# Optimization experiments

Hardware: AMD Instinct MI355X
Metric: run time of the kernel (lower is better)

## Reference

```python
import jax, jax.numpy as jnp
import numpy as np

D_MODEL = 1024
D_STATE = 16
LN_EPS = 1e-5


def setup_inputs() -> dict:
    key = jax.random.key(0)
    ks = jax.random.split(key, 10)
    B, L, D, N = 4, 1024, D_MODEL, D_STATE
    s = lambda fan_in: 1.0 / np.sqrt(fan_in)
    x_in = jax.random.normal(ks[0], (B, L, D), dtype=jnp.float32)
    W_in = jax.random.uniform(ks[1], (D, 2 * D), jnp.float32, -s(D), s(D))
    W_x = jax.random.uniform(ks[2], (D, D + 2 * N), jnp.float32, -s(D), s(D))
    W_dt = jax.random.uniform(ks[3], (D, D), jnp.float32, -s(D), s(D))
    b_dt = jax.random.uniform(ks[4], (D,), jnp.float32, -4.0, -1.0)
    A_log = jnp.tile(jnp.log(jnp.arange(1, N + 1, dtype=jnp.float32))[None, :], (D, 1))
    D_param = jnp.ones((D,), dtype=jnp.float32)
    W_out = jax.random.uniform(ks[5], (D, D), jnp.float32, -s(D), s(D))
    ln_g = jnp.ones((D,), dtype=jnp.float32)
    ln_b = jnp.zeros((D,), dtype=jnp.float32)
    return {"x_in": x_in, "W_in": W_in, "W_x": W_x, "W_dt": W_dt, "b_dt": b_dt,
            "A_log": A_log, "D_param": D_param, "W_out": W_out, "ln_g": ln_g, "ln_b": ln_b}


def reference(x_in, W_in, W_x, W_dt, b_dt, A_log, D_param, W_out, ln_g, ln_b):
    B, L, D = x_in.shape
    N = A_log.shape[1]
    xz = x_in @ W_in                       # [B,L,2D]
    x, z = xz[..., :D], xz[..., D:]
    proj = x @ W_x                         # [B,L,D+2N]
    delta_raw = proj[..., :D]
    B_ssm = proj[..., D:D + N]
    C_ssm = proj[..., D + N:]
    delta = jax.nn.softplus(delta_raw @ W_dt + b_dt)   # [B,L,D]
    A = -jnp.exp(A_log)                    # [D,N]
    dA = jnp.exp(jnp.einsum('bld,dn->bldn', delta, A))      # [B,L,D,N]
    dBx = jnp.einsum('bld,bln->bldn', delta * x, B_ssm)      # dB * x, fused

    def step(h, inp):
        dA_t, dBx_t, C_t = inp             # [B,D,N],[B,D,N],[B,N]
        h = dA_t * h + dBx_t
        y_t = jnp.einsum('bdn,bn->bd', h, C_t)
        return h, y_t

    h0 = jnp.zeros((B, D, N), dtype=x.dtype)
    xs = (jnp.moveaxis(dA, 1, 0), jnp.moveaxis(dBx, 1, 0), jnp.moveaxis(C_ssm, 1, 0))
    _, ys = jax.lax.scan(step, h0, xs)     # ys: [L,B,D]
    y = jnp.moveaxis(ys, 0, 1) + x * D_param
    y = (y * jax.nn.silu(z)) @ W_out
    res = y + x_in
    mu = jnp.mean(res, axis=-1, keepdims=True)
    var = jnp.var(res, axis=-1, keepdims=True)
    return (res - mu) * jax.lax.rsqrt(var + LN_EPS) * ln_g + ln_b
```

## Files before the change

kernel.cpp:

```cpp
#include <hip/hip_runtime.h>

#define D_MODEL 1024
#define D_STATE 16
#define M_ROWS  4096
#define SEQ_L   1024
#define NSEG    64
#define LSEG    16

typedef __bf16 bf16x8 __attribute__((ext_vector_type(8)));
typedef float  f32x4  __attribute__((ext_vector_type(4)));

__device__ __forceinline__ unsigned short f2bf(float f) {
  unsigned int u = __builtin_bit_cast(unsigned int, f);
  u += 0x7fffu + ((u >> 16) & 1u);
  return (unsigned short)(u >> 16);
}
__device__ __forceinline__ float bf2f(unsigned short b) {
  unsigned int u = ((unsigned int)b) << 16;
  return __builtin_bit_cast(float, u);
}
__device__ __forceinline__ float load_elem(const void* p, size_t i, int isbf) {
  if (isbf) return bf2f(((const unsigned short*)p)[i]);
  return ((const float*)p)[i];
}

__device__ __forceinline__ void gload16(const void* g, void* l) {
  typedef const __attribute__((address_space(1))) unsigned int GU;
  typedef __attribute__((address_space(3))) unsigned int LU;
  __builtin_amdgcn_global_load_lds((GU*)(unsigned long long)g,
                                   (LU*)(unsigned int)(unsigned long long)l,
                                   16, 0, 0);
}

__global__ void detect_kernel(const unsigned short* __restrict__ x, int* __restrict__ flag) {
  __shared__ int cnt;
  if (threadIdx.x == 0) cnt = 0;
  __syncthreads();
  unsigned int v = x[2 * threadIdx.x];
  unsigned int e = (v >> 7) & 0xFFu;
  int ok = (e >= 100u && e <= 135u) ? 1 : 0;
  atomicAdd(&cnt, ok);
  __syncthreads();
  if (threadIdx.x == 0) *flag = (cnt >= 128) ? 1 : 0;
}

__global__ void convert_x_kernel(const void* __restrict__ src,
                                 unsigned short* __restrict__ dstb,
                                 const int* __restrict__ flag) {
  int c = blockIdx.x * blockDim.x + threadIdx.x;
  int isbf = *flag;
  if (isbf) {
    ((uint4*)dstb)[c] = ((const uint4*)src)[c];
  } else {
    float4 a = ((const float4*)src)[2 * c];
    float4 b = ((const float4*)src)[2 * c + 1];
    uint4 p;
    p.x = (unsigned int)f2bf(a.x) | ((unsigned int)f2bf(a.y) << 16);
    p.y = (unsigned int)f2bf(a.z) | ((unsigned int)f2bf(a.w) << 16);
    p.z = (unsigned int)f2bf(b.x) | ((unsigned int)f2bf(b.y) << 16);
    p.w = (unsigned int)f2bf(b.z) | ((unsigned int)f2bf(b.w) << 16);
    ((uint4*)dstb)[c] = p;
  }
}

__global__ void convert_smalls_kernel(const void* b_dt, const void* A_log, const void* Dp,
                                      const void* ln_g, const void* ln_b,
                                      float* o_bdt, float* o_a2, float* o_dp,
                                      float* o_lng, float* o_lnb,
                                      const int* __restrict__ flag) {
  int g = blockIdx.x * blockDim.x + threadIdx.x;
  int isbf = *flag;
  if (g < 1024)              o_bdt[g]          = load_elem(b_dt, g, isbf);
  else if (g < 17408) {
    float v = load_elem(A_log, g - 1024, isbf);
    o_a2[g - 1024] = -expf(v) * 1.4426950408889634f;
  }
  else if (g < 18432)        o_dp[g - 17408]   = load_elem(Dp, g - 17408, isbf);
  else if (g < 19456)        o_lng[g - 18432]  = load_elem(ln_g, g - 18432, isbf);
  else                       o_lnb[g - 19456]  = load_elem(ln_b, g - 19456, isbf);
}

__global__ void transpose_all_kernel(const void* __restrict__ s0, const void* __restrict__ s1,
                                     const void* __restrict__ s2, const void* __restrict__ s3,
                                     unsigned short* __restrict__ d0, unsigned short* __restrict__ d1,
                                     unsigned short* __restrict__ d2, unsigned short* __restrict__ d3,
                                     const int* __restrict__ flag) {
  __shared__ float tile[32][33];
  const void* src; unsigned short* dst; int ncols, nx;
  switch (blockIdx.z) {
    case 0:  src = s0; dst = d0; ncols = 2048; nx = 64; break;
    case 1:  src = s1; dst = d1; ncols = 1056; nx = 33; break;
    case 2:  src = s2; dst = d2; ncols = 1024; nx = 32; break;
    default: src = s3; dst = d3; ncols = 1024; nx = 32; break;
  }
  if ((int)blockIdx.x >= nx) return;
  int tx = threadIdx.x, ty = threadIdx.y;
  int n0 = blockIdx.x * 32, k0 = blockIdx.y * 32;
  int isbf = *flag;
  #pragma unroll
  for (int r = 0; r < 4; ++r) {
    int k = k0 + ty + r * 8;
    int n = n0 + tx;
    float v = (n < ncols) ? load_elem(src, (size_t)k * ncols + n, isbf) : 0.f;
    tile[ty + r * 8][tx] = v;
  }
  __syncthreads();
  #pragma unroll
  for (int r = 0; r < 4; ++r) {
    int n = n0 + ty + r * 8;
    int k = k0 + tx;
    dst[(size_t)n * 1024 + k] = f2bf(tile[tx][ty + r * 8]);
  }
}

template<int MODE>
__global__ __launch_bounds__(256, 4) void gemm_bf(
    const unsigned short* __restrict__ A, const unsigned short* __restrict__ Bt, int ldb,
    void* __restrict__ o0, void* __restrict__ o1, void* __restrict__ o2,
    float* __restrict__ o3, float* __restrict__ o4,
    const float* __restrict__ aux, const void* __restrict__ auxv,
    const int* __restrict__ flag) {
  __shared__ __align__(16) unsigned short a_lds[3][64 * 32];
  __shared__ __align__(16) unsigned short b_lds[3][128 * 32];
  const int tid = threadIdx.x;
  const int m0 = blockIdx.x * 64, n0 = blockIdx.y * 128;
  const int wave = tid >> 6, lane = tid & 63;
  const int wr = (wave >> 1) * 32, wc = (wave & 1) * 64;
  const int lrow = lane & 15, quad = lane >> 4;

  const int sc = (lane & 3) ^ ((lane >> 3) & 3);
  const unsigned short* gA  = A  + (size_t)(m0 + wave * 16 + (lane >> 2)) * 1024 + sc * 8;
  const unsigned short* gB  = Bt + (size_t)(n0 + wave * 32 + (lane >> 2)) * ldb + sc * 8;
  const unsigned short* gB2 = gB + (size_t)16 * ldb;
  const int q2 = quad ^ ((lrow >> 1) & 3);

  f32x4 acc[2][4];
  #pragma unroll
  for (int i = 0; i < 2; ++i)
    #pragma unroll
    for (int j = 0; j < 4; ++j)
      #pragma unroll
      for (int r = 0; r < 4; ++r) acc[i][j][r] = 0.f;

  auto issue = [&](int k) {
    unsigned short* ab = a_lds[k % 3] + wave * 16 * 32;
    unsigned short* bb = b_lds[k % 3] + wave * 32 * 32;
    gload16(gA + k * 32, ab);
    gload16(gB + k * 32, bb);
    gload16(gB2 + k * 32, bb + 16 * 32);
  };
  auto compute = [&](int k) {
    const unsigned short* ard = a_lds[k % 3] + (wr + lrow) * 32 + q2 * 8;
    const unsigned short* brd = b_lds[k % 3] + (wc + lrow) * 32 + q2 * 8;
    bf16x8 af[2], bfr[4];
    #pragma unroll
    for (int i = 0; i < 2; ++i) af[i] = *(const bf16x8*)(ard + i * 16 * 32);
    #pragma unroll
    for (int j = 0; j < 4; ++j) bfr[j] = *(const bf16x8*)(brd + j * 16 * 32);
    #pragma unroll
    for (int i = 0; i < 2; ++i)
      #pragma unroll
      for (int j = 0; j < 4; ++j)
        acc[i][j] = __builtin_amdgcn_mfma_f32_16x16x32_bf16(af[i], bfr[j], acc[i][j], 0, 0, 0);
  };

  issue(0);
  issue(1);
  #pragma unroll
  for (int k = 0; k < 31; ++k) {
    asm volatile("s_waitcnt vmcnt(3)" ::: "memory");
    __builtin_amdgcn_s_barrier();
    if (k + 2 < 32) issue(k + 2);
    compute(k);
  }
  asm volatile("s_waitcnt vmcnt(0)" ::: "memory");
  __builtin_amdgcn_s_barrier();
  compute(31);

  const int isbf = (MODE == 4) ? *flag : 0;

  #pragma unroll
  for (int i = 0; i < 2; ++i) {
    #pragma unroll
    for (int jj = 0; jj < 4; ++jj) {
      #pragma unroll
      for (int r = 0; r < 4; ++r) {
        int m = m0 + wr + i * 16 + quad * 4 + r;
        int n = n0 + wc + jj * 16 + lrow;
        float v = acc[i][jj][r];
        if (MODE == 1) {
          if (n < 1024) {
            ((unsigned short*)o0)[(size_t)m * 1024 + n] = f2bf(v);
          } else {
            float sig = 1.f / (1.f + expf(-v));
            ((unsigned short*)o1)[(size_t)m * 1024 + (n - 1024)] = f2bf(v * sig);
          }
        } else if (MODE == 2) {
          if (n < 1024)       ((unsigned short*)o0)[(size_t)m * 1024 + n] = f2bf(v);
          else if (n < 1040)  o3[(size_t)m * D_STATE + (n - 1024)] = v;
          else if (n < 1056)  o4[(size_t)m * D_STATE + (n - 1040)] = v;
        } else if (MODE == 3) {
          float t = v + aux[n];
          float sp = (t > 20.f) ? t : log1pf(expf(t));
          ((unsigned short*)o0)[(size_t)m * 1024 + n] = f2bf(sp);
        } else {
          ((float*)o0)[(size_t)m * 1024 + n] =
              v + load_elem(auxv, (size_t)m * 1024 + n, isbf);
        }
      }
    }
  }
}

template<int PHASE>
__global__ __launch_bounds__(256) void scan_phase(
    const unsigned short* __restrict__ dl_bf, const unsigned short* __restrict__ x_bf,
    const unsigned short* __restrict__ z_bf, const float* __restrict__ Bs,
    const float* __restrict__ Cs, const float* __restrict__ A2g,
    const float* __restrict__ Dpar, const float* __restrict__ hinit,
    float* __restrict__ Hout, float* __restrict__ sdout,
    unsigned short* __restrict__ g) {
  __shared__ float4 bsh[LSEG][4];
  __shared__ float4 csh[LSEG][4];
  const int tid = threadIdx.x;
  const int bid = blockIdx.x;
  const int seg = bid >> 4;
  const int b = (bid >> 2) & 3;
  const int dc = bid & 3;
  const int d = dc * 256 + tid;
  const int t0 = seg * LSEG;
  const int bd = b * D_MODEL + d;

  if (tid < LSEG * 4) {
    int r = tid >> 2, q = tid & 3;
    size_t src = ((size_t)b * SEQ_L + t0 + r) * 4 + q;
    bsh[r][q] = ((const float4*)Bs)[src];
    if (PHASE == 1) csh[r][q] = ((const float4*)Cs)[src];
  }

  float A2r[16];
  {
    const float4* a4 = (const float4*)(A2g + (size_t)d * 16);
    #pragma unroll
    for (int q = 0; q < 4; ++q) {
      float4 v = a4[q];
      A2r[4*q] = v.x; A2r[4*q+1] = v.y; A2r[4*q+2] = v.z; A2r[4*q+3] = v.w;
    }
  }
  float h[16];
  if (PHASE == 1) {
    const float4* h4 = (const float4*)(hinit + (((size_t)seg * 4096) + bd) * 16);
    #pragma unroll
    for (int q = 0; q < 4; ++q) {
      float4 v = h4[q];
      h[4*q] = v.x; h[4*q+1] = v.y; h[4*q+2] = v.z; h[4*q+3] = v.w;
    }
  } else {
    #pragma unroll
    for (int n = 0; n < 16; ++n) h[n] = 0.f;
  }
  const float Dpd = (PHASE == 1) ? Dpar[d] : 0.f;
  float sd = 0.f;
  const size_t base = ((size_t)b * SEQ_L + t0) * D_MODEL + d;
  __syncthreads();

  unsigned short dreg[2][8], xreg[2][8], zreg[2][8];
  #pragma unroll
  for (int t = 0; t < 8; ++t) {
    size_t o = base + (size_t)t * D_MODEL;
    dreg[0][t] = dl_bf[o]; xreg[0][t] = x_bf[o];
    if (PHASE == 1) zreg[0][t] = z_bf[o];
  }
  #pragma unroll
  for (int c = 0; c < LSEG / 8; ++c) {
    const int cur = c & 1, nxt = cur ^ 1;
    if (c < LSEG / 8 - 1) {
      #pragma unroll
      for (int t = 0; t < 8; ++t) {
        size_t o = base + (size_t)((c + 1) * 8 + t) * D_MODEL;
        dreg[nxt][t] = dl_bf[o]; xreg[nxt][t] = x_bf[o];
        if (PHASE == 1) zreg[nxt][t] = z_bf[o];
      }
    }
    #pragma unroll
    for (int t = 0; t < 8; ++t) {
      const int tt = c * 8 + t;
      float dl = bf2f(dreg[cur][t]);
      float xx = bf2f(xreg[cur][t]);
      float dx = dl * xx;
      sd += dl;
      float4 b0 = bsh[tt][0], b1 = bsh[tt][1], b2 = bsh[tt][2], b3 = bsh[tt][3];
      float bb[16] = {b0.x,b0.y,b0.z,b0.w, b1.x,b1.y,b1.z,b1.w,
                      b2.x,b2.y,b2.z,b2.w, b3.x,b3.y,b3.z,b3.w};
      if (PHASE == 0) {
        #pragma unroll
        for (int n = 0; n < 16; ++n) {
          float dA = exp2f(dl * A2r[n]);
          h[n] = fmaf(dA, h[n], dx * bb[n]);
        }
      } else {
        float4 c0 = csh[tt][0], c1 = csh[tt][1], c2 = csh[tt][2], c3 = csh[tt][3];
        float cc[16] = {c0.x,c0.y,c0.z,c0.w, c1.x,c1.y,c1.z,c1.w,
                        c2.x,c2.y,c2.z,c2.w, c3.x,c3.y,c3.z,c3.w};
        float y = 0.f;
        #pragma unroll
        for (int n = 0; n < 16; ++n) {
          float dA = exp2f(dl * A2r[n]);
          h[n] = fmaf(dA, h[n], dx * bb[n]);
          y = fmaf(h[n], cc[n], y);
        }
        float zz = bf2f(zreg[cur][t]);
        g[base + (size_t)tt * D_MODEL] = f2bf(fmaf(xx, Dpd, y) * zz);
      }
    }
  }
  if (PHASE == 0) {
    float4* ho = (float4*)(Hout + (((size_t)seg * 4096) + bd) * 16);
    #pragma unroll
    for (int q = 0; q < 4; ++q)
      ho[q] = make_float4(h[4*q], h[4*q+1], h[4*q+2], h[4*q+3]);
    sdout[(size_t)seg * 4096 + bd] = sd;
  }
}

__global__ __launch_bounds__(256) void scan_phaseB(
    const float* __restrict__ H, const float* __restrict__ sdelta,
    const float* __restrict__ A2g, float* __restrict__ hinit) {
  int gidx = blockIdx.x * 256 + threadIdx.x;
  int bd = gidx >> 4, n = gidx & 15;
  float A2 = A2g[(size_t)(bd & (D_MODEL - 1)) * 16 + n];
  float hp = 0.f;
  for (int s = 0; s < NSEG; ++s) {
    size_t idx = ((size_t)s * 4096 + bd) * 16 + n;
    hinit[idx] = hp;
    float P = exp2f(A2 * sdelta[(size_t)s * 4096 + bd]);
    hp = fmaf(P, hp, H[idx]);
  }
}

__global__ __launch_bounds__(256) void ln_kernel(const float* __restrict__ res,
    const float* __restrict__ lng, const float* __restrict__ lnb,
    void* __restrict__ out, const int* __restrict__ flag) {
  int row = blockIdx.x, tid = threadIdx.x;
  const float4* r4 = (const float4*)(res + (size_t)row * D_MODEL);
  float4 v = r4[tid];
  float s = v.x + v.y + v.z + v.w;
  float q = v.x * v.x + v.y * v.y + v.z * v.z + v.w * v.w;
  #pragma unroll
  for (int m = 1; m < 64; m <<= 1) { s += __shfl_xor(s, m); q += __shfl_xor(q, m); }
  __shared__ float ss[4], qs[4];
  int w = tid >> 6;
  if ((tid & 63) == 0) { ss[w] = s; qs[w] = q; }
  __syncthreads();
  s = ss[0] + ss[1] + ss[2] + ss[3];
  q = qs[0] + qs[1] + qs[2] + qs[3];
  float mu = s * (1.f / D_MODEL);
  float var = q * (1.f / D_MODEL) - mu * mu;
  float rstd = rsqrtf(var + 1e-5f);
  float4 gg = ((const float4*)lng)[tid];
  float4 bb = ((const float4*)lnb)[tid];
  float o0 = (v.x - mu) * rstd * gg.x + bb.x;
  float o1 = (v.y - mu) * rstd * gg.y + bb.y;
  float o2 = (v.z - mu) * rstd * gg.z + bb.z;
  float o3 = (v.w - mu) * rstd * gg.w + bb.w;
  if (*flag) {
    ushort4 pv;
    pv.x = f2bf(o0); pv.y = f2bf(o1); pv.z = f2bf(o2); pv.w = f2bf(o3);
    ((ushort4*)out)[(size_t)row * 256 + tid] = pv;
  } else {
    ((float4*)out)[(size_t)row * 256 + tid] = make_float4(o0, o1, o2, o3);
  }
}

extern "C" void kernel_launch(void* const* d_in, const int* in_sizes, int n_in,
                              void* d_out, int out_size, void* d_ws, size_t ws_size,
                              hipStream_t stream) {
  (void)in_sizes; (void)n_in; (void)out_size; (void)ws_size;
  const void* x_in  = d_in[0];
  const void* W_in  = d_in[1];
  const void* W_x   = d_in[2];
  const void* W_dt  = d_in[3];
  const void* b_dt  = d_in[4];
  const void* A_log = d_in[5];
  const void* D_par = d_in[6];
  const void* W_out = d_in[7];
  const void* ln_g  = d_in[8];
  const void* ln_b  = d_in[9];

  char* ws = (char*)d_ws;
  size_t off = 0;
  auto alloc = [&](size_t bytes) -> void* {
    void* p = ws + off;
    off += (bytes + 255) & ~(size_t)255;
    return p;
  };
  int* flag               = (int*)alloc(16);
  unsigned short* x_in_b  = (unsigned short*)alloc((size_t)M_ROWS * D_MODEL * 2);
  float* bdt_f            = (float*)alloc(1024 * 4);
  float* a2_f             = (float*)alloc(16384 * 4);
  float* dp_f             = (float*)alloc(1024 * 4);
  float* lng_f            = (float*)alloc(1024 * 4);
  float* lnb_f            = (float*)alloc(1024 * 4);
  unsigned short* wt_in   = (unsigned short*)alloc((size_t)2048 * 1024 * 2);
  unsigned short* wt_x    = (unsigned short*)alloc((size_t)1152 * 1024 * 2);
  unsigned short* wt_dt   = (unsigned short*)alloc((size_t)1024 * 1024 * 2);
  unsigned short* wt_out  = (unsigned short*)alloc((size_t)1024 * 1024 * 2);
  unsigned short* x_bf    = (unsigned short*)alloc((size_t)M_ROWS * D_MODEL * 2);
  unsigned short* s_bf    = (unsigned short*)alloc((size_t)M_ROWS * D_MODEL * 2);
  unsigned short* draw_bf = (unsigned short*)alloc((size_t)M_ROWS * D_MODEL * 2);
  unsigned short* delta_bf= (unsigned short*)alloc((size_t)M_ROWS * D_MODEL * 2);
  float* bssm_f           = (float*)alloc((size_t)M_ROWS * D_STATE * 4);
  float* cssm_f           = (float*)alloc((size_t)M_ROWS * D_STATE * 4);
  float* H_f              = (float*)alloc((size_t)NSEG * 4096 * 16 * 4);
  float* hinit_f          = (float*)alloc((size_t)NSEG * 4096 * 16 * 4);
  float* sdelta_f         = (float*)alloc((size_t)NSEG * 4096 * 4);
  unsigned short* g_bf = draw_bf;
  float* res_f = (float*)x_bf;

  detect_kernel<<<1, 256, 0, stream>>>((const unsigned short*)x_in, flag);
  convert_x_kernel<<<2048, 256, 0, stream>>>(x_in, x_in_b, flag);
  convert_smalls_kernel<<<80, 256, 0, stream>>>(b_dt, A_log, D_par, ln_g, ln_b,
                                                bdt_f, a2_f, dp_f, lng_f, lnb_f, flag);
  dim3 tb(32, 8);
  transpose_all_kernel<<<dim3(64, 32, 4), tb, 0, stream>>>(
      W_in, W_x, W_dt, W_out, wt_in, wt_x, wt_dt, wt_out, flag);

  gemm_bf<1><<<dim3(64, 16), 256, 0, stream>>>(x_in_b, wt_in, 1024,
      x_bf, s_bf, nullptr, nullptr, nullptr, nullptr, nullptr, flag);
  gemm_bf<2><<<dim3(64, 9), 256, 0, stream>>>(x_bf, wt_x, 1024,
      draw_bf, nullptr, nullptr, bssm_f, cssm_f, nullptr, nullptr, flag);
  gemm_bf<3><<<dim3(64, 8), 256, 0, stream>>>(draw_bf, wt_dt, 1024,
      delta_bf, nullptr, nullptr, nullptr, nullptr, bdt_f, nullptr, flag);

  scan_phase<0><<<1024, 256, 0, stream>>>(delta_bf, x_bf, nullptr, bssm_f, nullptr,
                                          a2_f, nullptr, nullptr, H_f, sdelta_f, nullptr);
  scan_phaseB<<<256, 256, 0, stream>>>(H_f, sdelta_f, a2_f, hinit_f);
  scan_phase<1><<<1024, 256, 0, stream>>>(delta_bf, x_bf, s_bf, bssm_f, cssm_f,
                                          a2_f, dp_f, hinit_f, nullptr, nullptr, g_bf);

  gemm_bf<4><<<dim3(64, 8), 256, 0, stream>>>(g_bf, wt_out, 1024,
      res_f, nullptr, nullptr, nullptr, nullptr, nullptr, x_in, flag);
  ln_kernel<<<4096, 256, 0, stream>>>(res_f, lng_f, lnb_f, d_out, flag);
}
```

Baseline: 279.6 us.

## Precompute W_x·W_dt product to merge the delta GEMMs and fuse conversion kernels

Computes U = (W_x[:, :D] @ W_dt)^T once per call as a weight-only GEMM, then computes delta and the B/C projections from x in a single GEMM. This drops the separate delta_raw GEMM over all 4096 rows and its intermediate buffer. The dtype detection kernel is replaced by an inline wave ballot in each consumer, and the x and small-parameter conversions are merged into one launch. The weight product adds an extra bf16 rounding step compared with the two-stage path.

```diff
diff --git a/kernel.cpp b/kernel.cpp
--- a/kernel.cpp
+++ b/kernel.cpp
@@ -24,6 +24,13 @@
   return ((const float*)p)[i];
 }
 
+__device__ __forceinline__ int is_bf16(const void* x_in) {
+  unsigned int v = ((const unsigned short*)x_in)[2 * (threadIdx.x & 63)];
+  unsigned int e = (v >> 7) & 0xFFu;
+  unsigned long long m = __ballot(e >= 100u && e <= 135u);
+  return __popcll(m) >= 32;
+}
+
 __device__ __forceinline__ void gload16(const void* g, void* l) {
   typedef const __attribute__((address_space(1))) unsigned int GU;
   typedef __attribute__((address_space(3))) unsigned int LU;
@@ -32,71 +39,62 @@
                                    16, 0, 0);
 }
 
-__global__ void detect_kernel(const unsigned short* __restrict__ x, int* __restrict__ flag) {
-  __shared__ int cnt;
-  if (threadIdx.x == 0) cnt = 0;
-  __syncthreads();
-  unsigned int v = x[2 * threadIdx.x];
-  unsigned int e = (v >> 7) & 0xFFu;
-  int ok = (e >= 100u && e <= 135u) ? 1 : 0;
-  atomicAdd(&cnt, ok);
-  __syncthreads();
-  if (threadIdx.x == 0) *flag = (cnt >= 128) ? 1 : 0;
-}
-
-__global__ void convert_x_kernel(const void* __restrict__ src,
-                                 unsigned short* __restrict__ dstb,
-                                 const int* __restrict__ flag) {
-  int c = blockIdx.x * blockDim.x + threadIdx.x;
-  int isbf = *flag;
-  if (isbf) {
-    ((uint4*)dstb)[c] = ((const uint4*)src)[c];
+__global__ void convert_kernel(const void* __restrict__ x_in,
+                               unsigned short* __restrict__ x_b,
+                               const void* __restrict__ W_x,
+                               unsigned short* __restrict__ wx_raw,
+                               const void* b_dt, const void* A_log, const void* Dp,
+                               const void* ln_g, const void* ln_b,
+                               float* o_bdt, float* o_a2, float* o_dp,
+                               float* o_lng, float* o_lnb) {
+  const int isbf = is_bf16(x_in);
+  const int bid = blockIdx.x;
+  if (bid < 2048 || bid >= 2128) {
+    const void* src; unsigned short* dst; int c;
+    if (bid < 2048) { src = x_in; dst = x_b; c = bid * 256 + threadIdx.x; }
+    else { src = W_x; dst = wx_raw; c = (bid - 2128) * 256 + threadIdx.x; }
+    if (isbf) {
+      ((uint4*)dst)[c] = ((const uint4*)src)[c];
+    } else {
+      float4 a = ((const float4*)src)[2 * c];
+      float4 b = ((const float4*)src)[2 * c + 1];
+      uint4 p;
+      p.x = (unsigned int)f2bf(a.x) | ((unsigned int)f2bf(a.y) << 16);
+      p.y = (unsigned int)f2bf(a.z) | ((unsigned int)f2bf(a.w) << 16);
+      p.z = (unsigned int)f2bf(b.x) | ((unsigned int)f2bf(b.y) << 16);
+      p.w = (unsigned int)f2bf(b.z) | ((unsigned int)f2bf(b.w) << 16);
+      ((uint4*)dst)[c] = p;
+    }
   } else {
-    float4 a = ((const float4*)src)[2 * c];
-    float4 b = ((const float4*)src)[2 * c + 1];
-    uint4 p;
-    p.x = (unsigned int)f2bf(a.x) | ((unsigned int)f2bf(a.y) << 16);
-    p.y = (unsigned int)f2bf(a.z) | ((unsigned int)f2bf(a.w) << 16);
-    p.z = (unsigned int)f2bf(b.x) | ((unsigned int)f2bf(b.y) << 16);
-    p.w = (unsigned int)f2bf(b.z) | ((unsigned int)f2bf(b.w) << 16);
-    ((uint4*)dstb)[c] = p;
-  }
-}
-
-__global__ void convert_smalls_kernel(const void* b_dt, const void* A_log, const void* Dp,
-                                      const void* ln_g, const void* ln_b,
-                                      float* o_bdt, float* o_a2, float* o_dp,
-                                      float* o_lng, float* o_lnb,
-                                      const int* __restrict__ flag) {
-  int g = blockIdx.x * blockDim.x + threadIdx.x;
-  int isbf = *flag;
-  if (g < 1024)              o_bdt[g]          = load_elem(b_dt, g, isbf);
-  else if (g < 17408) {
-    float v = load_elem(A_log, g - 1024, isbf);
-    o_a2[g - 1024] = -expf(v) * 1.4426950408889634f;
-  }
-  else if (g < 18432)        o_dp[g - 17408]   = load_elem(Dp, g - 17408, isbf);
-  else if (g < 19456)        o_lng[g - 18432]  = load_elem(ln_g, g - 18432, isbf);
-  else                       o_lnb[g - 19456]  = load_elem(ln_b, g - 19456, isbf);
+    int g = (bid - 2048) * 256 + threadIdx.x;
+    if (g < 1024)              o_bdt[g]          = load_elem(b_dt, g, isbf);
+    else if (g < 17408) {
+      float v = load_elem(A_log, g - 1024, isbf);
+      o_a2[g - 1024] = -expf(v) * 1.4426950408889634f;
+    }
+    else if (g < 18432)        o_dp[g - 17408]   = load_elem(Dp, g - 17408, isbf);
+    else if (g < 19456)        o_lng[g - 18432]  = load_elem(ln_g, g - 18432, isbf);
+    else                       o_lnb[g - 19456]  = load_elem(ln_b, g - 19456, isbf);
+  }
 }
 
 __global__ void transpose_all_kernel(const void* __restrict__ s0, const void* __restrict__ s1,
                                      const void* __restrict__ s2, const void* __restrict__ s3,
                                      unsigned short* __restrict__ d0, unsigned short* __restrict__ d1,
                                      unsigned short* __restrict__ d2, unsigned short* __restrict__ d3,
-                                     const int* __restrict__ flag) {
+                                     const void* __restrict__ x_in) {
   __shared__ float tile[32][33];
-  const void* src; unsigned short* dst; int ncols, nx;
+  const int isbf = is_bf16(x_in);
+  const void* src; unsigned short* dst; int ncols, col0, nx;
   switch (blockIdx.z) {
-    case 0:  src = s0; dst = d0; ncols = 2048; nx = 64; break;
-    case 1:  src = s1; dst = d1; ncols = 1056; nx = 33; break;
-    case 2:  src = s2; dst = d2; ncols = 1024; nx = 32; break;
-    default: src = s3; dst = d3; ncols = 1024; nx = 32; break;
+    case 0:  src = s0; dst = d0; ncols = 2048; col0 = 0;    nx = 64; break;
+    case 1:  src = s1; dst = d1; ncols = 1056; col0 = 1024; nx = 4;  break;
+    case 2:  src = s2; dst = d2; ncols = 1024; col0 = 0;    nx = 32; break;
+    default: src = s3; dst = d3; ncols = 1024; col0 = 0;    nx = 32; break;
   }
   if ((int)blockIdx.x >= nx) return;
   int tx = threadIdx.x, ty = threadIdx.y;
-  int n0 = blockIdx.x * 32, k0 = blockIdx.y * 32;
-  int isbf = *flag;
+  int n0 = col0 + blockIdx.x * 32, k0 = blockIdx.y * 32;
   #pragma unroll
   for (int r = 0; r < 4; ++r) {
     int k = k0 + ty + r * 8;
@@ -109,7 +107,7 @@
   for (int r = 0; r < 4; ++r) {
     int n = n0 + ty + r * 8;
     int k = k0 + tx;
-    dst[(size_t)n * 1024 + k] = f2bf(tile[tx][ty + r * 8]);
+    dst[(size_t)(n - col0) * 1024 + k] = f2bf(tile[tx][ty + r * 8]);
   }
 }
 
@@ -118,19 +116,23 @@
     const unsigned short* __restrict__ A, const unsigned short* __restrict__ Bt, int ldb,
     void* __restrict__ o0, void* __restrict__ o1, void* __restrict__ o2,
     float* __restrict__ o3, float* __restrict__ o4,
-    const float* __restrict__ aux, const void* __restrict__ auxv,
-    const int* __restrict__ flag) {
+    const float* __restrict__ aux, const void* __restrict__ auxv) {
   __shared__ __align__(16) unsigned short a_lds[3][64 * 32];
   __shared__ __align__(16) unsigned short b_lds[3][128 * 32];
+  const int isbf = (MODE == 4) ? is_bf16(auxv) : 0;
   const int tid = threadIdx.x;
   const int m0 = blockIdx.x * 64, n0 = blockIdx.y * 128;
   const int wave = tid >> 6, lane = tid & 63;
   const int wr = (wave >> 1) * 32, wc = (wave & 1) * 64;
   const int lrow = lane & 15, quad = lane >> 4;
 
+  const unsigned short* Bsrc = Bt;
+  int nb0 = n0;
+  if (MODE == 2 && n0 >= 1024) { Bsrc = (const unsigned short*)o2; nb0 = n0 - 1024; }
+
   const int sc = (lane & 3) ^ ((lane >> 3) & 3);
-  const unsigned short* gA  = A  + (size_t)(m0 + wave * 16 + (lane >> 2)) * 1024 + sc * 8;
-  const unsigned short* gB  = Bt + (size_t)(n0 + wave * 32 + (lane >> 2)) * ldb + sc * 8;
+  const unsigned short* gA  = A    + (size_t)(m0 + wave * 16 + (lane >> 2)) * 1024 + sc * 8;
+  const unsigned short* gB  = Bsrc + (size_t)(nb0 + wave * 32 + (lane >> 2)) * ldb + sc * 8;
   const unsigned short* gB2 = gB + (size_t)16 * ldb;
   const int q2 = quad ^ ((lrow >> 1) & 3);
 
@@ -177,8 +179,6 @@
   __builtin_amdgcn_s_barrier();
   compute(31);
 
-  const int isbf = (MODE == 4) ? *flag : 0;
-
   #pragma unroll
   for (int i = 0; i < 2; ++i) {
     #pragma unroll
@@ -188,7 +188,9 @@
         int m = m0 + wr + i * 16 + quad * 4 + r;
         int n = n0 + wc + jj * 16 + lrow;
         float v = acc[i][jj][r];
-        if (MODE == 1) {
+        if (MODE == 0) {
+          ((unsigned short*)o0)[(size_t)m * 1024 + n] = f2bf(v);
+        } else if (MODE == 1) {
           if (n < 1024) {
             ((unsigned short*)o0)[(size_t)m * 1024 + n] = f2bf(v);
           } else {
@@ -196,13 +198,13 @@
             ((unsigned short*)o1)[(size_t)m * 1024 + (n - 1024)] = f2bf(v * sig);
           }
         } else if (MODE == 2) {
-          if (n < 1024)       ((unsigned short*)o0)[(size_t)m * 1024 + n] = f2bf(v);
+          if (n < 1024) {
+            float t = v + aux[n];
+            float sp = (t > 20.f) ? t : log1pf(expf(t));
+            ((unsigned short*)o0)[(size_t)m * 1024 + n] = f2bf(sp);
+          }
           else if (n < 1040)  o3[(size_t)m * D_STATE + (n - 1024)] = v;
           else if (n < 1056)  o4[(size_t)m * D_STATE + (n - 1040)] = v;
-        } else if (MODE == 3) {
-          float t = v + aux[n];
-          float sp = (t > 20.f) ? t : log1pf(expf(t));
-          ((unsigned short*)o0)[(size_t)m * 1024 + n] = f2bf(sp);
         } else {
           ((float*)o0)[(size_t)m * 1024 + n] =
               v + load_elem(auxv, (size_t)m * 1024 + n, isbf);
@@ -330,6 +332,7 @@
   int bd = gidx >> 4, n = gidx & 15;
   float A2 = A2g[(size_t)(bd & (D_MODEL - 1)) * 16 + n];
   float hp = 0.f;
+  #pragma unroll 8
   for (int s = 0; s < NSEG; ++s) {
     size_t idx = ((size_t)s * 4096 + bd) * 16 + n;
     hinit[idx] = hp;
@@ -340,7 +343,8 @@
 
 __global__ __launch_bounds__(256) void ln_kernel(const float* __restrict__ res,
     const float* __restrict__ lng, const float* __restrict__ lnb,
-    void* __restrict__ out, const int* __restrict__ flag) {
+    void* __restrict__ out, const void* __restrict__ x_in) {
+  const int isbf = is_bf16(x_in);
   int row = blockIdx.x, tid = threadIdx.x;
   const float4* r4 = (const float4*)(res + (size_t)row * D_MODEL);
   float4 v = r4[tid];
@@ -363,7 +367,7 @@
   float o1 = (v.y - mu) * rstd * gg.y + bb.y;
   float o2 = (v.z - mu) * rstd * gg.z + bb.z;
   float o3 = (v.w - mu) * rstd * gg.w + bb.w;
-  if (*flag) {
+  if (isbf) {
     ushort4 pv;
     pv.x = f2bf(o0); pv.y = f2bf(o1); pv.z = f2bf(o2); pv.w = f2bf(o3);
     ((ushort4*)out)[(size_t)row * 256 + tid] = pv;
@@ -394,43 +398,44 @@
     off += (bytes + 255) & ~(size_t)255;
     return p;
   };
-  int* flag               = (int*)alloc(16);
   unsigned short* x_in_b  = (unsigned short*)alloc((size_t)M_ROWS * D_MODEL * 2);
+  unsigned short* wx_raw  = (unsigned short*)alloc((size_t)1024 * 1056 * 2);
   float* bdt_f            = (float*)alloc(1024 * 4);
   float* a2_f             = (float*)alloc(16384 * 4);
   float* dp_f             = (float*)alloc(1024 * 4);
   float* lng_f            = (float*)alloc(1024 * 4);
   float* lnb_f            = (float*)alloc(1024 * 4);
   unsigned short* wt_in   = (unsigned short*)alloc((size_t)2048 * 1024 * 2);
-  unsigned short* wt_x    = (unsigned short*)alloc((size_t)1152 * 1024 * 2);
+  unsigned short* wt_xbc  = (unsigned short*)alloc((size_t)128 * 1024 * 2);
   unsigned short* wt_dt   = (unsigned short*)alloc((size_t)1024 * 1024 * 2);
   unsigned short* wt_out  = (unsigned short*)alloc((size_t)1024 * 1024 * 2);
+  unsigned short* U_bf    = (unsigned short*)alloc((size_t)1024 * 1024 * 2);
   unsigned short* x_bf    = (unsigned short*)alloc((size_t)M_ROWS * D_MODEL * 2);
   unsigned short* s_bf    = (unsigned short*)alloc((size_t)M_ROWS * D_MODEL * 2);
-  unsigned short* draw_bf = (unsigned short*)alloc((size_t)M_ROWS * D_MODEL * 2);
   unsigned short* delta_bf= (unsigned short*)alloc((size_t)M_ROWS * D_MODEL * 2);
+  unsigned short* g_bf    = (unsigned short*)alloc((size_t)M_ROWS * D_MODEL * 2);
   float* bssm_f           = (float*)alloc((size_t)M_ROWS * D_STATE * 4);
   float* cssm_f           = (float*)alloc((size_t)M_ROWS * D_STATE * 4);
   float* H_f              = (float*)alloc((size_t)NSEG * 4096 * 16 * 4);
   float* hinit_f          = (float*)alloc((size_t)NSEG * 4096 * 16 * 4);
   float* sdelta_f         = (float*)alloc((size_t)NSEG * 4096 * 4);
-  unsigned short* g_bf = draw_bf;
   float* res_f = (float*)x_bf;
 
-  detect_kernel<<<1, 256, 0, stream>>>((const unsigned short*)x_in, flag);
-  convert_x_kernel<<<2048, 256, 0, stream>>>(x_in, x_in_b, flag);
-  convert_smalls_kernel<<<80, 256, 0, stream>>>(b_dt, A_log, D_par, ln_g, ln_b,
-                                                bdt_f, a2_f, dp_f, lng_f, lnb_f, flag);
+  convert_kernel<<<2656, 256, 0, stream>>>(x_in, x_in_b, W_x, wx_raw,
+                                           b_dt, A_log, D_par, ln_g, ln_b,
+                                           bdt_f, a2_f, dp_f, lng_f, lnb_f);
   dim3 tb(32, 8);
   transpose_all_kernel<<<dim3(64, 32, 4), tb, 0, stream>>>(
-      W_in, W_x, W_dt, W_out, wt_in, wt_x, wt_dt, wt_out, flag);
+      W_in, W_x, W_dt, W_out, wt_in, wt_xbc, wt_dt, wt_out, x_in);
+
+  gemm_bf<0><<<dim3(16, 8), 256, 0, stream>>>(wt_dt, wx_raw, 1056,
+      U_bf, nullptr, nullptr, nullptr, nullptr, nullptr, nullptr);
 
   gemm_bf<1><<<dim3(64, 16), 256, 0, stream>>>(x_in_b, wt_in, 1024,
-      x_bf, s_bf, nullptr, nullptr, nullptr, nullptr, nullptr, flag);
-  gemm_bf<2><<<dim3(64, 9), 256, 0, stream>>>(x_bf, wt_x, 1024,
-      draw_bf, nullptr, nullptr, bssm_f, cssm_f, nullptr, nullptr, flag);
-  gemm_bf<3><<<dim3(64, 8), 256, 0, stream>>>(draw_bf, wt_dt, 1024,
-      delta_bf, nullptr, nullptr, nullptr, nullptr, bdt_f, nullptr, flag);
+      x_bf, s_bf, nullptr, nullptr, nullptr, nullptr, nullptr);
+
+  gemm_bf<2><<<dim3(64, 9), 256, 0, stream>>>(x_bf, U_bf, 1024,
+      delta_bf, nullptr, wt_xbc, bssm_f, cssm_f, bdt_f, nullptr);
 
   scan_phase<0><<<1024, 256, 0, stream>>>(delta_bf, x_bf, nullptr, bssm_f, nullptr,
                                           a2_f, nullptr, nullptr, H_f, sdelta_f, nullptr);
@@ -439,6 +444,7 @@
                                           a2_f, dp_f, hinit_f, nullptr, nullptr, g_bf);
 
   gemm_bf<4><<<dim3(64, 8), 256, 0, stream>>>(g_bf, wt_out, 1024,
-      res_f, nullptr, nullptr, nullptr, nullptr, nullptr, x_in, flag);
-  ln_kernel<<<4096, 256, 0, stream>>>(res_f, lng_f, lnb_f, d_out, flag);
-}
+      res_f, nullptr, nullptr, nullptr, nullptr, nullptr, x_in);
+
+  ln_kernel<<<4096, 256, 0, stream>>>(res_f, lng_f, lnb_f, d_out, x_in);
+}
```

Result: faster. 266.3 us (-4.7%).
